# Performance work log

Hardware: AMD Instinct MI355X
Metric: run time of the kernel (lower is better)

The kernel has to match this reference:

```python
import jax, jax.numpy as jnp
import numpy as np

N_NODES = 100000
EMB_DIM = 128
N_LAYERS = 3
N_EDGES = 1600000


def setup_inputs() -> dict:
    key = jax.random.key(0)
    ks = jax.random.split(key, 6)
    edge_index = jax.random.randint(ks[0], (2, N_EDGES), 0, N_NODES, dtype=jnp.int32)
    deg_inv = jax.random.uniform(ks[1], (N_NODES,), dtype=jnp.float32)
    node_emb = 0.02 * jax.random.normal(ks[2], (N_NODES, EMB_DIM), dtype=jnp.float32)
    W = jax.random.normal(ks[3], (N_LAYERS, EMB_DIM, EMB_DIM), dtype=jnp.float32) / np.sqrt(EMB_DIM)
    b = jnp.zeros((N_LAYERS, EMB_DIM), dtype=jnp.float32)
    gamma = jnp.ones((EMB_DIM,), dtype=jnp.float32)
    beta = jnp.zeros((EMB_DIM,), dtype=jnp.float32)
    return {"edge_index": edge_index, "deg_inv": deg_inv, "node_emb": node_emb,
            "W": W, "b": b, "gamma": gamma, "beta": beta}


def reference(edge_index, deg_inv, node_emb, W, b, gamma, beta):
    src, dst = edge_index[0], edge_index[1]
    x = node_emb  # [N, d]
    for l in range(N_LAYERS):
        # scatter-add neighbor aggregation: m[v] = sum_{(u->v)} x[u]
        m = jax.ops.segment_sum(x[src], dst, num_segments=N_NODES)  # [N, d]
        m = m * deg_inv[:, None]
        h = jax.nn.gelu(m @ W[l] + b[l], approximate=False)  # dropout=0 (eval)
        x = x + h  # residual
    # LayerNorm over feature dim
    mu = jnp.mean(x, axis=-1, keepdims=True)
    var = jnp.var(x, axis=-1, keepdims=True)
    x = (x - mu) * jax.lax.rsqrt(var + 1e-5) * gamma + beta
    return x
```

## Files before the change

kernel.cpp:

```cpp
#include <hip/hip_runtime.h>
#include <hip/hip_bf16.h>
#include <math.h>

#define N_NODES 100000
#define EMB 128
#define N_EDGES 1600000
#define N_LAYERS 3

#define NB 400
#define NPB 250
#define CAP 8192
#define CAPB 6144
#define BSTR 16
#define EPT 8
#define BUCKET_THREADS 512
#define BUCKET_BLOCKS ((N_EDGES + BUCKET_THREADS * EPT - 1) / (BUCKET_THREADS * EPT))

typedef __bf16 bf16x8 __attribute__((ext_vector_type(8)));
typedef float f32x4 __attribute__((ext_vector_type(4)));


__global__ __launch_bounds__(BUCKET_THREADS) void bucket_kernel(
    const int* __restrict__ src, const int* __restrict__ dst,
    int* __restrict__ bcur, unsigned* __restrict__ pairs) {
  __shared__ int scnt[NB];
  __shared__ int sbase[NB];
  const int t = threadIdx.x;
  if (t < NB) scnt[t] = 0;
  __syncthreads();
  unsigned pk[EPT];
  int bk[EPT], lofs[EPT];
  const int base_e = blockIdx.x * BUCKET_THREADS * EPT;
#pragma unroll
  for (int it = 0; it < EPT; ++it) {
    int i = base_e + it * BUCKET_THREADS + t;
    bk[it] = -1;
    if (i < N_EDGES) {
      int d = dst[i];
      int s = src[i];
      int b = d / NPB;
      int vloc = d - b * NPB;
      bk[it] = b;
      pk[it] = ((unsigned)vloc << 17) | (unsigned)s;
      lofs[it] = atomicAdd(&scnt[b], 1);
    }
  }
  __syncthreads();
  if (t < NB) sbase[t] = atomicAdd(&bcur[t * BSTR], scnt[t]);
  __syncthreads();
#pragma unroll
  for (int it = 0; it < EPT; ++it) {
    if (bk[it] >= 0) {
      int idx = sbase[bk[it]] + lofs[it];
      if (idx < CAP) pairs[(size_t)bk[it] * CAP + idx] = pk[it];
    }
  }
}

__device__ __forceinline__ int* scan512(int* pin, int* pout, int t) {
  for (int off = 1; off < 512; off <<= 1) {
    for (int i = t; i < 512; i += 256) {
      int v = pin[i];
      if (i >= off) v += pin[i - off];
      pout[i] = v;
    }
    __syncthreads();
    int* tmp = pin; pin = pout; pout = tmp;
  }
  return pin;
}

__global__ __launch_bounds__(256) void fillb_kernel(const unsigned* __restrict__ pairs,
                                                    const int* __restrict__ bcur,
                                                    int* __restrict__ row_ptr,
                                                    int* __restrict__ col) {
  __shared__ int sA[512], sB[512];
  __shared__ int cnt[NPB], cur[NPB];
  __shared__ unsigned pstage[CAPB];
  __shared__ int colstage[CAPB];
  const int t = threadIdx.x;
  const int b = blockIdx.x;

  for (int i = t; i < 512; i += 256) sA[i] = (i < NB) ? bcur[i * BSTR] : 0;
  __syncthreads();
  int* r = scan512(sA, sB, t);
  int base_b = b ? r[b - 1] : 0;
  int n = r[b] - base_b;
  if (n > CAP) n = CAP;
  const unsigned* pg = pairs + (size_t)b * CAP;
  const bool fits = (n <= CAPB);

  if (fits) for (int i = t; i < n; i += 256) pstage[i] = pg[i];
  if (t < NPB) cnt[t] = 0;
  __syncthreads();
  for (int i = t; i < n; i += 256) atomicAdd(&cnt[(fits ? pstage[i] : pg[i]) >> 17], 1);
  __syncthreads();
  for (int i = t; i < 512; i += 256) sA[i] = (i < NPB) ? cnt[i] : 0;
  __syncthreads();
  r = scan512(sA, sB, t);
  if (t < NPB) {
    int ex = r[t] - cnt[t];
    row_ptr[b * NPB + t] = base_b + ex;
    cur[t] = ex;
  }
  if (b == NB - 1 && t == 0) row_ptr[N_NODES] = N_EDGES;
  __syncthreads();
  for (int i = t; i < n; i += 256) {
    unsigned p = fits ? pstage[i] : pg[i];
    int pos = atomicAdd(&cur[p >> 17], 1);
    int s = (int)(p & 0x1FFFFu);
    if (fits) colstage[pos] = s;
    else col[base_b + pos] = s;
  }
  __syncthreads();
  if (fits) for (int i = t; i < n; i += 256) col[base_b + i] = colstage[i];
}


__global__ __launch_bounds__(256) void tobf16_kernel(const float* __restrict__ in,
                                                     __hip_bfloat16* __restrict__ xb) {
  size_t i = (size_t)blockIdx.x * 256 + threadIdx.x;
  const float4* p = (const float4*)in + i * 2;
  float4 a = p[0], b = p[1];
  union { __hip_bfloat16 h[8]; uint4 u; } r;
  r.h[0] = __float2bfloat16(a.x); r.h[1] = __float2bfloat16(a.y);
  r.h[2] = __float2bfloat16(a.z); r.h[3] = __float2bfloat16(a.w);
  r.h[4] = __float2bfloat16(b.x); r.h[5] = __float2bfloat16(b.y);
  r.h[6] = __float2bfloat16(b.z); r.h[7] = __float2bfloat16(b.w);
  ((uint4*)xb)[i] = r.u;
}

__global__ __launch_bounds__(256) void wt_kernel(const float* __restrict__ W,
                                                 __hip_bfloat16* __restrict__ WT) {
  int l = blockIdx.x;
  const float* Wl = W + (size_t)l * EMB * EMB;
  __hip_bfloat16* WTl = WT + (size_t)l * EMB * EMB;
  for (int i = threadIdx.x; i < EMB * EMB; i += 256) {
    int k = i >> 7, c = i & 127;
    WTl[c * EMB + k] = __float2bfloat16(Wl[i]);
  }
}


__device__ __forceinline__ float bf_lo(unsigned int w) { return __uint_as_float(w << 16); }
__device__ __forceinline__ float bf_hi(unsigned int w) { return __uint_as_float(w & 0xFFFF0000u); }

__device__ __forceinline__ float gelu_exact(float v) {
  return 0.5f * v * (1.f + erff(v * 0.70710678118654752f));
}

template <int LAST>
__global__ __launch_bounds__(1024, 8) void fused_kernel(
    const __hip_bfloat16* __restrict__ xb_in,
    const int* __restrict__ row_ptr,
    const int* __restrict__ col,
    const float* __restrict__ deg_inv,
    const __hip_bfloat16* __restrict__ WTl,
    const float* __restrict__ bias,
    __hip_bfloat16* __restrict__ xb_out,
    float* __restrict__ xf_out,
    const float* __restrict__ gamma,
    const float* __restrict__ beta) {
  __shared__ __hip_bfloat16 sM[32][136];
  __shared__ float sX[LAST ? 32 * 129 : 1];

  const int t = threadIdx.x;
  const int w = t >> 6;
  const int lane = t & 63;
  const int q = lane >> 4;
  const int l15 = lane & 15;
  const int row0b = blockIdx.x * 32;

  const char* gbase = (const char*)xb_in + l15 * 16;
  for (int nn = 0; nn < 2; ++nn) {
    const int v = __builtin_amdgcn_readfirstlane(row0b + w * 2 + nn);
    const int beg = row_ptr[v], end = row_ptr[v + 1];
    float a0 = 0.f, a1 = 0.f, a2 = 0.f, a3 = 0.f, a4 = 0.f, a5 = 0.f, a6 = 0.f, a7 = 0.f;
#define ACC8(W) { a0 += bf_lo(W.x); a1 += bf_hi(W.x); a2 += bf_lo(W.y); a3 += bf_hi(W.y); \
                  a4 += bf_lo(W.z); a5 += bf_hi(W.z); a6 += bf_lo(W.w); a7 += bf_hi(W.w); }
    int e = beg;
    for (; e + 16 <= end; e += 16) {
      int u0 = col[e + q];
      int u1 = col[e + 4 + q];
      int u2 = col[e + 8 + q];
      int u3 = col[e + 12 + q];
      uint4 w0 = *(const uint4*)(gbase + (size_t)u0 * 256);
      uint4 w1 = *(const uint4*)(gbase + (size_t)u1 * 256);
      uint4 w2 = *(const uint4*)(gbase + (size_t)u2 * 256);
      uint4 w3 = *(const uint4*)(gbase + (size_t)u3 * 256);
      ACC8(w0) ACC8(w1) ACC8(w2) ACC8(w3)
    }
    for (; e < end; e += 4) {
      int idx = e + q;
      bool valid = idx < end;
      int u = col[valid ? idx : beg];
      uint4 w0 = *(const uint4*)(gbase + (size_t)u * 256);
      if (valid) ACC8(w0)
    }
#undef ACC8
    a0 += __shfl_xor(a0, 16, 64); a0 += __shfl_xor(a0, 32, 64);
    a1 += __shfl_xor(a1, 16, 64); a1 += __shfl_xor(a1, 32, 64);
    a2 += __shfl_xor(a2, 16, 64); a2 += __shfl_xor(a2, 32, 64);
    a3 += __shfl_xor(a3, 16, 64); a3 += __shfl_xor(a3, 32, 64);
    a4 += __shfl_xor(a4, 16, 64); a4 += __shfl_xor(a4, 32, 64);
    a5 += __shfl_xor(a5, 16, 64); a5 += __shfl_xor(a5, 32, 64);
    a6 += __shfl_xor(a6, 16, 64); a6 += __shfl_xor(a6, 32, 64);
    a7 += __shfl_xor(a7, 16, 64); a7 += __shfl_xor(a7, 32, 64);
    if (q == 0) {
      float di = deg_inv[v];
      union { __hip_bfloat16 h[8]; uint4 u4; } r;
      r.h[0] = __float2bfloat16(a0 * di); r.h[1] = __float2bfloat16(a1 * di);
      r.h[2] = __float2bfloat16(a2 * di); r.h[3] = __float2bfloat16(a3 * di);
      r.h[4] = __float2bfloat16(a4 * di); r.h[5] = __float2bfloat16(a5 * di);
      r.h[6] = __float2bfloat16(a6 * di); r.h[7] = __float2bfloat16(a7 * di);
      *(uint4*)(&sM[w * 2 + nn][l15 * 8]) = r.u4;
    }
  }

  const int rh = w >> 3;
  const int ct8 = w & 7;
  bf16x8 bfr[4];
  {
    const __hip_bfloat16* wp = WTl + (size_t)(ct8 * 16 + l15) * EMB + q * 8;
#pragma unroll
    for (int ks = 0; ks < 4; ++ks)
      bfr[ks] = *(const bf16x8*)(wp + ks * 32);
  }
  __syncthreads();

  f32x4 acc = (f32x4)(0.f);
#pragma unroll
  for (int ks = 0; ks < 4; ++ks) {
    bf16x8 af = *(const bf16x8*)(&sM[rh * 16 + l15][q * 8 + ks * 32]);
    acc = __builtin_amdgcn_mfma_f32_16x16x32_bf16(af, bfr[ks], acc, 0, 0, 0);
  }

  {
    const int colg = ct8 * 16 + l15;
    const float bb = bias[colg];
#pragma unroll
    for (int j = 0; j < 4; ++j) {
      const int rloc = rh * 16 + q * 4 + j;
      const size_t off = (size_t)(row0b + rloc) * EMB + colg;
      float xv = __bfloat162float(xb_in[off]) + gelu_exact(acc[j] + bb);
      if (!LAST) xb_out[off] = __float2bfloat16(xv);
      else sX[rloc * 129 + colg] = xv;
    }
  }

  if (LAST) {
    __syncthreads();
    float g1 = gamma[lane], g2 = gamma[lane + 64];
    float b1 = beta[lane], b2 = beta[lane + 64];
    for (int rr = 0; rr < 2; ++rr) {
      int r = w * 2 + rr;
      float v1 = sX[r * 129 + lane], v2 = sX[r * 129 + lane + 64];
      float s = v1 + v2;
      float sq = fmaf(v1, v1, v2 * v2);
      for (int off = 1; off < 64; off <<= 1) {
        s += __shfl_xor(s, off, 64);
        sq += __shfl_xor(sq, off, 64);
      }
      float mu = s * (1.f / EMB);
      float var = sq * (1.f / EMB) - mu * mu;
      float rstd = rsqrtf(var + 1e-5f);
      size_t rowoff = (size_t)(row0b + r) * EMB;
      xf_out[rowoff + lane] = (v1 - mu) * rstd * g1 + b1;
      xf_out[rowoff + lane + 64] = (v2 - mu) * rstd * g2 + b2;
    }
  }
}


extern "C" void kernel_launch(void* const* d_in, const int* in_sizes, int n_in,
                              void* d_out, int out_size, void* d_ws, size_t ws_size,
                              hipStream_t stream) {
  const int* edge_index = (const int*)d_in[0];
  const float* deg_inv = (const float*)d_in[1];
  const float* node_emb = (const float*)d_in[2];
  const float* W = (const float*)d_in[3];
  const float* b = (const float*)d_in[4];
  const float* gamma = (const float*)d_in[5];
  const float* beta = (const float*)d_in[6];
  const int* src = edge_index;
  const int* dst = edge_index + N_EDGES;
  float* x = (float*)d_out;

  char* ws = (char*)d_ws;
  auto take = [&](size_t bytes) {
    char* p = ws;
    ws += (bytes + 255) & ~(size_t)255;
    return p;
  };
  __hip_bfloat16* xbA = (__hip_bfloat16*)take((size_t)N_NODES * EMB * 2);
  __hip_bfloat16* xbB = (__hip_bfloat16*)take((size_t)N_NODES * EMB * 2);
  __hip_bfloat16* WT = (__hip_bfloat16*)take((size_t)N_LAYERS * EMB * EMB * 2);
  int* row_ptr = (int*)take((N_NODES + 1) * sizeof(int));
  int* col = (int*)take(N_EDGES * sizeof(int));
  int* bcur = (int*)take(NB * BSTR * sizeof(int));
  unsigned* pairs = (unsigned*)xbB;

  hipMemsetAsync(bcur, 0, NB * BSTR * sizeof(int), stream);

  tobf16_kernel<<<N_NODES * EMB / 8 / 256, 256, 0, stream>>>(node_emb, xbA);
  wt_kernel<<<N_LAYERS, 256, 0, stream>>>(W, WT);

  bucket_kernel<<<BUCKET_BLOCKS, BUCKET_THREADS, 0, stream>>>(src, dst, bcur, pairs);
  fillb_kernel<<<NB, 256, 0, stream>>>(pairs, bcur, row_ptr, col);

  const int NBLK = N_NODES / 32;
  fused_kernel<0><<<NBLK, 1024, 0, stream>>>(xbA, row_ptr, col, deg_inv,
                                             WT, b, xbB, nullptr, nullptr, nullptr);
  fused_kernel<0><<<NBLK, 1024, 0, stream>>>(xbB, row_ptr, col, deg_inv,
                                             WT + (size_t)EMB * EMB, b + EMB,
                                             xbA, nullptr, nullptr, nullptr);
  fused_kernel<1><<<NBLK, 1024, 0, stream>>>(xbA, row_ptr, col, deg_inv,
                                             WT + (size_t)2 * EMB * EMB, b + 2 * EMB,
                                             nullptr, x, gamma, beta);
}
```

Before: 315.7 us.

## Process 16 nodes per block with one wave per node and coalesced epilogue

```diff
diff --git a/kernel.cpp b/kernel.cpp
--- a/kernel.cpp
+++ b/kernel.cpp
@@ -161,19 +161,18 @@
     float* __restrict__ xf_out,
     const float* __restrict__ gamma,
     const float* __restrict__ beta) {
-  __shared__ __hip_bfloat16 sM[32][136];
-  __shared__ float sX[LAST ? 32 * 129 : 1];
+  __shared__ __hip_bfloat16 sM[16][136];
 
   const int t = threadIdx.x;
   const int w = t >> 6;
   const int lane = t & 63;
   const int q = lane >> 4;
   const int l15 = lane & 15;
-  const int row0b = blockIdx.x * 32;
+  const int row0b = blockIdx.x * 16;
 
   const char* gbase = (const char*)xb_in + l15 * 16;
-  for (int nn = 0; nn < 2; ++nn) {
-    const int v = __builtin_amdgcn_readfirstlane(row0b + w * 2 + nn);
+  {
+    const int v = __builtin_amdgcn_readfirstlane(row0b + w);
     const int beg = row_ptr[v], end = row_ptr[v + 1];
     float a0 = 0.f, a1 = 0.f, a2 = 0.f, a3 = 0.f, a4 = 0.f, a5 = 0.f, a6 = 0.f, a7 = 0.f;
 #define ACC8(W) { a0 += bf_lo(W.x); a1 += bf_hi(W.x); a2 += bf_lo(W.y); a3 += bf_hi(W.y); \
@@ -213,15 +212,13 @@
       r.h[2] = __float2bfloat16(a2 * di); r.h[3] = __float2bfloat16(a3 * di);
       r.h[4] = __float2bfloat16(a4 * di); r.h[5] = __float2bfloat16(a5 * di);
       r.h[6] = __float2bfloat16(a6 * di); r.h[7] = __float2bfloat16(a7 * di);
-      *(uint4*)(&sM[w * 2 + nn][l15 * 8]) = r.u4;
-    }
-  }
-
-  const int rh = w >> 3;
-  const int ct8 = w & 7;
+      *(uint4*)(&sM[w][l15 * 8]) = r.u4;
+    }
+  }
+
   bf16x8 bfr[4];
-  {
-    const __hip_bfloat16* wp = WTl + (size_t)(ct8 * 16 + l15) * EMB + q * 8;
+  if (w < 8) {
+    const __hip_bfloat16* wp = WTl + (size_t)(w * 16 + l15) * EMB + q * 8;
 #pragma unroll
     for (int ks = 0; ks < 4; ++ks)
       bfr[ks] = *(const bf16x8*)(wp + ks * 32);
@@ -229,32 +226,35 @@
   __syncthreads();
 
   f32x4 acc = (f32x4)(0.f);
-#pragma unroll
-  for (int ks = 0; ks < 4; ++ks) {
-    bf16x8 af = *(const bf16x8*)(&sM[rh * 16 + l15][q * 8 + ks * 32]);
-    acc = __builtin_amdgcn_mfma_f32_16x16x32_bf16(af, bfr[ks], acc, 0, 0, 0);
-  }
+  if (w < 8) {
+#pragma unroll
+    for (int ks = 0; ks < 4; ++ks) {
+      bf16x8 af = *(const bf16x8*)(&sM[l15][q * 8 + ks * 32]);
+      acc = __builtin_amdgcn_mfma_f32_16x16x32_bf16(af, bfr[ks], acc, 0, 0, 0);
+    }
+  }
+  __syncthreads();
+  if (w < 8) {
+    const int colg = w * 16 + l15;
+    const float bb = bias[colg];
+#pragma unroll
+    for (int j = 0; j < 4; ++j)
+      sM[q * 4 + j][colg] = __float2bfloat16(gelu_exact(acc[j] + bb));
+  }
+  __syncthreads();
 
   {
-    const int colg = ct8 * 16 + l15;
-    const float bb = bias[colg];
-#pragma unroll
-    for (int j = 0; j < 4; ++j) {
-      const int rloc = rh * 16 + q * 4 + j;
-      const size_t off = (size_t)(row0b + rloc) * EMB + colg;
-      float xv = __bfloat162float(xb_in[off]) + gelu_exact(acc[j] + bb);
-      if (!LAST) xb_out[off] = __float2bfloat16(xv);
-      else sX[rloc * 129 + colg] = xv;
-    }
-  }
-
-  if (LAST) {
-    __syncthreads();
-    float g1 = gamma[lane], g2 = gamma[lane + 64];
-    float b1 = beta[lane], b2 = beta[lane + 64];
-    for (int rr = 0; rr < 2; ++rr) {
-      int r = w * 2 + rr;
-      float v1 = sX[r * 129 + lane], v2 = sX[r * 129 + lane + 64];
+    const size_t rowoff = (size_t)(row0b + w) * EMB;
+    unsigned rg = *(const unsigned*)(&sM[w][lane * 2]);
+    unsigned rr = *(const unsigned*)((const char*)xb_in + (rowoff + lane * 2) * 2);
+    float v1 = bf_lo(rr) + bf_lo(rg);
+    float v2 = bf_hi(rr) + bf_hi(rg);
+    if (!LAST) {
+      union { __hip_bfloat16 h[2]; unsigned u; } o;
+      o.h[0] = __float2bfloat16(v1);
+      o.h[1] = __float2bfloat16(v2);
+      *(unsigned*)((char*)xb_out + (rowoff + lane * 2) * 2) = o.u;
+    } else {
       float s = v1 + v2;
       float sq = fmaf(v1, v1, v2 * v2);
       for (int off = 1; off < 64; off <<= 1) {
@@ -264,9 +264,12 @@
       float mu = s * (1.f / EMB);
       float var = sq * (1.f / EMB) - mu * mu;
       float rstd = rsqrtf(var + 1e-5f);
-      size_t rowoff = (size_t)(row0b + r) * EMB;
-      xf_out[rowoff + lane] = (v1 - mu) * rstd * g1 + b1;
-      xf_out[rowoff + lane + 64] = (v2 - mu) * rstd * g2 + b2;
+      float2 g = *(const float2*)(gamma + lane * 2);
+      float2 be = *(const float2*)(beta + lane * 2);
+      float2 o;
+      o.x = (v1 - mu) * rstd * g.x + be.x;
+      o.y = (v2 - mu) * rstd * g.y + be.y;
+      *(float2*)(xf_out + rowoff + lane * 2) = o;
     }
   }
 }
@@ -308,7 +311,7 @@
   bucket_kernel<<<BUCKET_BLOCKS, BUCKET_THREADS, 0, stream>>>(src, dst, bcur, pairs);
   fillb_kernel<<<NB, 256, 0, stream>>>(pairs, bcur, row_ptr, col);
 
-  const int NBLK = N_NODES / 32;
+  const int NBLK = N_NODES / 16;
   fused_kernel<0><<<NBLK, 1024, 0, stream>>>(xbA, row_ptr, col, deg_inv,
                                              WT, b, xbB, nullptr, nullptr, nullptr);
   fused_kernel<0><<<NBLK, 1024, 0, stream>>>(xbB, row_ptr, col, deg_inv,
```

Result: slower. 328.9 us (+4.2%).
